# Kernel tuning notes

Hardware: AMD Instinct MI355X
Metric: run time of the kernel (lower is better)

## Reference

```python
import jax, jax.numpy as jnp
import numpy as np

N = 100000   # nodes
E = 3200000  # edges
C = 256      # in_channels
H = 64       # hidden_channels
G = 512      # graphs in batch
FC = [128, 64, 32, 16]
OUT = 2
EPS = 1e-5


def _linear(key, fan_in, fan_out):
    k1, k2 = jax.random.split(key)
    s = 1.0 / np.sqrt(fan_in)
    W = jax.random.uniform(k1, (fan_in, fan_out), jnp.float32, -s, s)
    b = jax.random.uniform(k2, (fan_out,), jnp.float32, -s, s)
    return W, b


def setup_inputs() -> dict:
    key = jax.random.key(0)
    ks = jax.random.split(key, 12)
    x = jax.random.normal(ks[0], (N, C), jnp.float32)
    edge_index = jax.random.randint(ks[1], (2, E), 0, N, dtype=jnp.int64)
    batch = jnp.sort(jax.random.randint(ks[2], (N,), 0, G, dtype=jnp.int64))
    w1, b1 = _linear(ks[3], C, H)
    w2, b2 = _linear(ks[4], H, H)
    g1 = jnp.ones((H,), jnp.float32); be1 = jnp.zeros((H,), jnp.float32)
    g2 = jnp.ones((H,), jnp.float32); be2 = jnp.zeros((H,), jnp.float32)
    fw1, fb1 = _linear(ks[5], H, FC[0])
    fw2, fb2 = _linear(ks[6], FC[0], FC[1])
    fw3, fb3 = _linear(ks[7], FC[1], FC[2])
    fw4, fb4 = _linear(ks[8], FC[2], FC[3])
    ow, ob = _linear(ks[9], FC[3], OUT)
    return dict(x=x, edge_index=edge_index, batch=batch,
                w1=w1, b1=b1, w2=w2, b2=b2,
                g1=g1, be1=be1, g2=g2, be2=be2,
                fw1=fw1, fb1=fb1, fw2=fw2, fb2=fb2,
                fw3=fw3, fb3=fb3, fw4=fw4, fb4=fb4,
                ow=ow, ob=ob)


def _gcn_layers(x, edge_index, w1, b1, w2, b2, g1, be1, g2, be2):
    # PyG GCNConv: add self loops, symmetric deg^-1/2 normalization, scatter-add at dst
    loops = jnp.arange(N, dtype=edge_index.dtype)
    src = jnp.concatenate([edge_index[0], loops])
    dst = jnp.concatenate([edge_index[1], loops])
    deg = jax.ops.segment_sum(jnp.ones((E + N,), jnp.float32), dst, num_segments=N)
    dis = jnp.where(deg > 0, jax.lax.rsqrt(jnp.maximum(deg, 1.0)), 0.0)
    norm = (dis[src] * dis[dst])[:, None]  # [E+N, 1]

    def conv(h, W, b):
        h = h @ W
        return jax.ops.segment_sum(h[src] * norm, dst, num_segments=N) + b

    def bn(h, g, be):  # BatchNorm1d over node dim (training-mode batch stats)
        m = jnp.mean(h, axis=0)
        v = jnp.var(h, axis=0)
        return (h - m) * jax.lax.rsqrt(v + EPS) * g + be

    h = bn(jax.nn.relu(conv(x, w1, b1)), g1, be1)   # dropout = identity (eval)
    h = bn(jax.nn.relu(conv(h, w2, b2)), g2, be2)
    return h


def reference(x, edge_index, batch, w1, b1, w2, b2, g1, be1, g2, be2,
              fw1, fb1, fw2, fb2, fw3, fb3, fw4, fb4, ow, ob):
    h = _gcn_layers(x, edge_index, w1, b1, w2, b2, g1, be1, g2, be2)
    # global_mean_pool over batch vector
    s = jax.ops.segment_sum(h, batch, num_segments=G)
    cnt = jax.ops.segment_sum(jnp.ones((N,), jnp.float32), batch, num_segments=G)
    p = s / jnp.maximum(cnt, 1.0)[:, None]  # [G, H]
    h = jax.nn.relu(p @ fw1 + fb1)
    h = jax.nn.relu(h @ fw2 + fb2)
    h = jax.nn.relu(h @ fw3 + fb3)
    h = jax.nn.relu(h @ fw4 + fb4)
    return h @ ow + ob  # [G, OUT]
```

## Files before the change

kernel.cpp:

```cpp
#include <hip/hip_runtime.h>
#include <hip/hip_fp16.h>

#define N_NODES 100000
#define E_EDGES 3200000
#define NG      512
#define BN_EPS  1e-5f

#define BSH     7
#define BNODES  128
#define NBUCK   782
#define NCHUNK  1024
#define CHUNK   3125

__global__ __launch_bounds__(256) void k_zero(float* __restrict__ stats1,
                                              float* __restrict__ stats2,
                                              float* __restrict__ sums,
                                              float* __restrict__ cnt) {
  int i = blockIdx.x * 256 + threadIdx.x;
  if (i < 128) { stats1[i] = 0.f; stats2[i] = 0.f; }
  if (i < NG * 64) sums[i] = 0.f;
  if (i < NG) cnt[i] = 0.f;
}

__global__ __launch_bounds__(256) void kb_hist(const int* __restrict__ ei,
                                               int* __restrict__ counts) {
  __shared__ int h[NBUCK];
  const int c = blockIdx.x, tid = threadIdx.x;
  for (int b = tid; b < NBUCK; b += 256) h[b] = 0;
  __syncthreads();
  const int* dst = ei + E_EDGES + c * CHUNK;
  for (int i = tid; i < CHUNK; i += 256) atomicAdd(&h[dst[i] >> BSH], 1);
  __syncthreads();
  for (int b = tid; b < NBUCK; b += 256) counts[b * NCHUNK + c] = h[b];
}

__global__ __launch_bounds__(1024) void kb_scan1(int* __restrict__ counts,
                                                 int* __restrict__ btot) {
  __shared__ int sm[NCHUNK];
  const int b = blockIdx.x, tid = threadIdx.x;
  const int cval = counts[b * NCHUNK + tid];
  int val = cval;
  sm[tid] = val;
  __syncthreads();
  for (int off = 1; off < NCHUNK; off <<= 1) {
    int t = (tid >= off) ? sm[tid - off] : 0;
    __syncthreads();
    val += t;
    sm[tid] = val;
    __syncthreads();
  }
  counts[b * NCHUNK + tid] = val - cval;
  if (tid == NCHUNK - 1) btot[b] = val;
}

__global__ __launch_bounds__(1024) void kb_scan2(const int* __restrict__ btot,
                                                 int* __restrict__ bbase) {
  __shared__ int sm[1024];
  const int tid = threadIdx.x;
  const int cval = (tid < NBUCK) ? btot[tid] : 0;
  int val = cval;
  sm[tid] = val;
  __syncthreads();
  for (int off = 1; off < 1024; off <<= 1) {
    int t = (tid >= off) ? sm[tid - off] : 0;
    __syncthreads();
    val += t;
    sm[tid] = val;
    __syncthreads();
  }
  if (tid < NBUCK) bbase[tid] = val - cval;
  if (tid == NBUCK - 1) bbase[NBUCK] = val;
}

__global__ __launch_bounds__(256) void kb_scatter(const int* __restrict__ ei,
                                                  const int* __restrict__ counts,
                                                  const int* __restrict__ bbase,
                                                  int* __restrict__ binned) {
  __shared__ int cur[NBUCK];
  const int c = blockIdx.x, tid = threadIdx.x;
  for (int b = tid; b < NBUCK; b += 256) cur[b] = bbase[b] + counts[b * NCHUNK + c];
  __syncthreads();
  const int* srcp = ei + c * CHUNK;
  const int* dstp = ei + E_EDGES + c * CHUNK;
  for (int i = tid; i < CHUNK; i += 256) {
    const int s = srcp[i], d = dstp[i];
    const int pos = atomicAdd(&cur[d >> BSH], 1);
    binned[pos] = ((d & (BNODES - 1)) << 17) | s;
  }
}

__global__ __launch_bounds__(256) void kb_degsort(const int* __restrict__ binned,
                                                  const int* __restrict__ bbase,
                                                  int* __restrict__ csr,
                                                  int* __restrict__ row_start,
                                                  float* __restrict__ dis) {
  __shared__ int h[BNODES];
  __shared__ int pre[BNODES];
  const int b = blockIdx.x, tid = threadIdx.x;
  if (tid < BNODES) h[tid] = 0;
  __syncthreads();
  const int e0 = bbase[b], e1 = bbase[b + 1];
  for (int i = e0 + tid; i < e1; i += 256) atomicAdd(&h[binned[i] >> 17], 1);
  __syncthreads();
  if (tid < BNODES) pre[tid] = h[tid];
  __syncthreads();
  for (int off = 1; off < BNODES; off <<= 1) {
    int t = (tid >= off && tid < BNODES) ? pre[tid - off] : 0;
    __syncthreads();
    if (tid < BNODES) pre[tid] += t;
    __syncthreads();
  }
  if (tid < BNODES) {
    const int n = b * BNODES + tid;
    const int ex = e0 + pre[tid] - h[tid];
    if (n < N_NODES) {
      row_start[n] = ex;
      dis[n] = rsqrtf((float)(h[tid] + 1));
    }
    h[tid] = ex;
  }
  if (b == NBUCK - 1 && tid == 0) row_start[N_NODES] = E_EDGES;
  __syncthreads();
  for (int i = e0 + tid; i < e1; i += 256) {
    const int v = binned[i];
    const int pos = atomicAdd(&h[v >> 17], 1);
    csr[pos] = v & 0x1FFFF;
  }
}

template <int K, bool BN>
__global__ __launch_bounds__(256) void k_gemm(const float* __restrict__ in,
                                              const float* __restrict__ W,
                                              const float* __restrict__ dis,
                                              const float* __restrict__ stats,
                                              const float* __restrict__ gam,
                                              const float* __restrict__ bet,
                                              __half* __restrict__ y) {
  __shared__ float xs[64 * 68];
  __shared__ float wsm[64 * 64];
  __shared__ float scv[64], shv[64];
  const int tid = threadIdx.x;
  const int n0 = blockIdx.x * 64;
  const int lane = tid & 63, wv = tid >> 6;
  const int nq = lane & 15;
  const int chb = wv * 16 + (lane >> 4) * 4;
  if (BN) {
    if (tid < 64) {
      const float m = stats[tid] * (1.0f / N_NODES);
      const float v = stats[64 + tid] * (1.0f / N_NODES) - m * m;
      const float sc = rsqrtf(v + BN_EPS) * gam[tid];
      scv[tid] = sc;
      shv[tid] = bet[tid] - m * sc;
    }
  }
  float a[4][4] = {{0,0,0,0},{0,0,0,0},{0,0,0,0},{0,0,0,0}};
  for (int c0 = 0; c0 < K; c0 += 64) {
    __syncthreads();
#pragma unroll
    for (int i = 0; i < 4; ++i) {
      const int idx = tid + i * 256;
      const int n = idx >> 4, c4 = (idx & 15) * 4;
      const int nn = min(n0 + n, N_NODES - 1);
      float4 v = *(const float4*)&in[(size_t)nn * K + c0 + c4];
      if (BN) {
        v.x = v.x * scv[c4] + shv[c4];
        v.y = v.y * scv[c4 + 1] + shv[c4 + 1];
        v.z = v.z * scv[c4 + 2] + shv[c4 + 2];
        v.w = v.w * scv[c4 + 3] + shv[c4 + 3];
      }
      *(float4*)&xs[n * 68 + c4] = v;
    }
#pragma unroll
    for (int i = 0; i < 4; ++i) {
      const int idx = tid + i * 256;
      const int c = idx >> 4, ch4 = (idx & 15) * 4;
      *(float4*)&wsm[c * 64 + ch4] = *(const float4*)&W[(size_t)(c0 + c) * 64 + ch4];
    }
    __syncthreads();
    for (int c = 0; c < 64; c += 4) {
      float wq[4][4];
#pragma unroll
      for (int cc = 0; cc < 4; ++cc) {
        const float4 w4 = *(const float4*)&wsm[(c + cc) * 64 + chb];
        wq[cc][0] = w4.x; wq[cc][1] = w4.y; wq[cc][2] = w4.z; wq[cc][3] = w4.w;
      }
#pragma unroll
      for (int i = 0; i < 4; ++i) {
        const float4 xv = *(const float4*)&xs[(nq + 16 * i) * 68 + c];
#pragma unroll
        for (int j = 0; j < 4; ++j) {
          a[i][j] = fmaf(xv.x, wq[0][j],
                    fmaf(xv.y, wq[1][j],
                    fmaf(xv.z, wq[2][j],
                    fmaf(xv.w, wq[3][j], a[i][j]))));
        }
      }
    }
  }
#pragma unroll
  for (int i = 0; i < 4; ++i) {
    const int n = n0 + nq + 16 * i;
    if (n < N_NODES) {
      const float d = dis[n];
      union { __half h[4]; float2 f; } u;
      u.h[0] = __float2half_rn(d * a[i][0]);
      u.h[1] = __float2half_rn(d * a[i][1]);
      u.h[2] = __float2half_rn(d * a[i][2]);
      u.h[3] = __float2half_rn(d * a[i][3]);
      *(float2*)&y[(size_t)n * 64 + chb] = u.f;
    }
  }
}

template <bool POOL>
__global__ __launch_bounds__(256) void k_gather(const int* __restrict__ csr,
                                                const int* __restrict__ rs,
                                                const __half* __restrict__ y,
                                                const float* __restrict__ dis,
                                                const float* __restrict__ bias,
                                                float* __restrict__ hout,
                                                float* __restrict__ stats,
                                                const int* __restrict__ batch,
                                                float* __restrict__ sums,
                                                float* __restrict__ cnt) {
  const int tid = threadIdx.x;
  const int lane = tid & 63;
  const int p = lane >> 5;
  const int c = lane & 31;
  const int wid = (blockIdx.x * 256 + tid) >> 6;
  const int nw = (gridDim.x * 256) >> 6;
  const int per = (N_NODES + nw - 1) / nw;
  const int n0 = wid * per;
  const int n1 = min(N_NODES, n0 + per);
  const float bx = bias[2 * c], by = bias[2 * c + 1];
  float s1x = 0.f, s1y = 0.f, s2x = 0.f, s2y = 0.f;
  int curg = -1, run = 0;
  float px = 0.f, py = 0.f;
  for (int n = n0; n < n1; ++n) {
    int e = rs[n];
    const int end = rs[n + 1];
    float ax = 0.f, ay = 0.f;
    if (p == 0) {
      const float2 f = __half22float2(*(const __half2*)&y[(size_t)n * 64 + 2 * c]);
      ax = f.x; ay = f.y;
    }
    for (; e + 8 <= end; e += 8) {
      const int i0 = csr[e + p];
      const int i1 = csr[e + 2 + p];
      const int i2 = csr[e + 4 + p];
      const int i3 = csr[e + 6 + p];
      const float2 f0 = __half22float2(*(const __half2*)&y[(size_t)i0 * 64 + 2 * c]);
      const float2 f1 = __half22float2(*(const __half2*)&y[(size_t)i1 * 64 + 2 * c]);
      const float2 f2 = __half22float2(*(const __half2*)&y[(size_t)i2 * 64 + 2 * c]);
      const float2 f3 = __half22float2(*(const __half2*)&y[(size_t)i3 * 64 + 2 * c]);
      ax += (f0.x + f1.x) + (f2.x + f3.x);
      ay += (f0.y + f1.y) + (f2.y + f3.y);
    }
    for (; e + 2 <= end; e += 2) {
      const int i0 = csr[e + p];
      const float2 f = __half22float2(*(const __half2*)&y[(size_t)i0 * 64 + 2 * c]);
      ax += f.x; ay += f.y;
    }
    if (e < end && p == 0) {
      const int i0 = csr[e];
      const float2 f = __half22float2(*(const __half2*)&y[(size_t)i0 * 64 + 2 * c]);
      ax += f.x; ay += f.y;
    }
    ax += __shfl_xor(ax, 32);
    ay += __shfl_xor(ay, 32);
    const float d = dis[n];
    const float vx = fmaxf(d * ax + bx, 0.f);
    const float vy = fmaxf(d * ay + by, 0.f);
    if (lane < 32) {
      if (!POOL) *(float2*)&hout[(size_t)n * 64 + 2 * c] = make_float2(vx, vy);
      s1x += vx; s1y += vy;
      s2x += vx * vx; s2y += vy * vy;
    }
    if (POOL) {
      const int g = batch[n];
      if (g != curg) {
        if (run) {
          if (lane < 32) {
            atomicAdd(&sums[curg * 64 + 2 * c], px);
            atomicAdd(&sums[curg * 64 + 2 * c + 1], py);
          }
          if (lane == 0) atomicAdd(&cnt[curg], (float)run);
        }
        curg = g; run = 0; px = 0.f; py = 0.f;
      }
      if (lane < 32) { px += vx; py += vy; }
      ++run;
    }
  }
  if (POOL && run) {
    if (lane < 32) {
      atomicAdd(&sums[curg * 64 + 2 * c], px);
      atomicAdd(&sums[curg * 64 + 2 * c + 1], py);
    }
    if (lane == 0) atomicAdd(&cnt[curg], (float)run);
  }
  __shared__ float r1[256], r2[256];
  const int wv = tid >> 6;
  if (lane < 32) {
    r1[wv * 64 + 2 * c] = s1x; r1[wv * 64 + 2 * c + 1] = s1y;
    r2[wv * 64 + 2 * c] = s2x; r2[wv * 64 + 2 * c + 1] = s2y;
  }
  __syncthreads();
  if (tid < 64) {
    atomicAdd(&stats[tid], r1[tid] + r1[tid + 64] + r1[tid + 128] + r1[tid + 192]);
  } else if (tid < 128) {
    const int h = tid - 64;
    atomicAdd(&stats[64 + h], r2[h] + r2[h + 64] + r2[h + 128] + r2[h + 192]);
  }
}

__global__ __launch_bounds__(128) void k_mlp(const float* __restrict__ sums,
                                             const float* __restrict__ cnt,
                                             const float* __restrict__ stats,
                                             const float* __restrict__ gam,
                                             const float* __restrict__ bet,
                                             const float* __restrict__ fw1, const float* __restrict__ fb1,
                                             const float* __restrict__ fw2, const float* __restrict__ fb2,
                                             const float* __restrict__ fw3, const float* __restrict__ fb3,
                                             const float* __restrict__ fw4, const float* __restrict__ fb4,
                                             const float* __restrict__ ow, const float* __restrict__ ob,
                                             float* __restrict__ out) {
  __shared__ float u0[128], u1[128];
  const int g = blockIdx.x, t = threadIdx.x;
  if (t < 64) {
    const float m = stats[t] * (1.0f / N_NODES);
    const float v = stats[64 + t] * (1.0f / N_NODES) - m * m;
    const float sc = rsqrtf(v + BN_EPS) * gam[t];
    const float sh = bet[t] - m * sc;
    u0[t] = (sums[g * 64 + t] / fmaxf(cnt[g], 1.0f)) * sc + sh;
  }
  __syncthreads();
  if (t < 128) {
    float a = fb1[t];
    for (int k = 0; k < 64; ++k) a = fmaf(u0[k], fw1[k * 128 + t], a);
    u1[t] = fmaxf(a, 0.f);
  }
  __syncthreads();
  if (t < 64) {
    float a = fb2[t];
    for (int k = 0; k < 128; ++k) a = fmaf(u1[k], fw2[k * 64 + t], a);
    u0[t] = fmaxf(a, 0.f);
  }
  __syncthreads();
  if (t < 32) {
    float a = fb3[t];
    for (int k = 0; k < 64; ++k) a = fmaf(u0[k], fw3[k * 32 + t], a);
    u1[t] = fmaxf(a, 0.f);
  }
  __syncthreads();
  if (t < 16) {
    float a = fb4[t];
    for (int k = 0; k < 32; ++k) a = fmaf(u1[k], fw4[k * 16 + t], a);
    u0[t] = fmaxf(a, 0.f);
  }
  __syncthreads();
  if (t < 2) {
    float a = ob[t];
    for (int k = 0; k < 16; ++k) a = fmaf(u0[k], ow[k * 2 + t], a);
    out[g * 2 + t] = a;
  }
}

extern "C" void kernel_launch(void* const* d_in, const int* in_sizes, int n_in,
                              void* d_out, int out_size, void* d_ws, size_t ws_size,
                              hipStream_t stream) {
  const float* x    = (const float*)d_in[0];
  const int*   ei   = (const int*)d_in[1];
  const int*   batch= (const int*)d_in[2];
  const float* w1   = (const float*)d_in[3];
  const float* b1   = (const float*)d_in[4];
  const float* w2   = (const float*)d_in[5];
  const float* b2   = (const float*)d_in[6];
  const float* g1   = (const float*)d_in[7];
  const float* be1  = (const float*)d_in[8];
  const float* g2   = (const float*)d_in[9];
  const float* be2  = (const float*)d_in[10];
  const float* fw1  = (const float*)d_in[11]; const float* fb1 = (const float*)d_in[12];
  const float* fw2  = (const float*)d_in[13]; const float* fb2 = (const float*)d_in[14];
  const float* fw3  = (const float*)d_in[15]; const float* fb3 = (const float*)d_in[16];
  const float* fw4  = (const float*)d_in[17]; const float* fb4 = (const float*)d_in[18];
  const float* ow   = (const float*)d_in[19]; const float* ob  = (const float*)d_in[20];
  float* out = (float*)d_out;

  char* ws = (char*)d_ws;
  auto alloc = [&](size_t bytes) {
    void* p = ws;
    ws += (bytes + 255) & ~(size_t)255;
    return p;
  };
  float*  dis      = (float*)alloc((size_t)N_NODES * 4);
  int*    counts   = (int*)  alloc((size_t)NBUCK * NCHUNK * 4);
  int*    btot     = (int*)  alloc((size_t)NBUCK * 4);
  int*    bbase    = (int*)  alloc((size_t)(NBUCK + 1) * 4);
  int*    binned   = (int*)  alloc((size_t)E_EDGES * 4);
  int*    csr      = (int*)  alloc((size_t)E_EDGES * 4);
  int*    row_start= (int*)  alloc((size_t)(N_NODES + 1) * 4);
  __half* yH       = (__half*)alloc((size_t)N_NODES * 64 * 2);
  float*  hB       = (float*)alloc((size_t)N_NODES * 64 * 4);
  float*  stats1   = (float*)alloc(512);
  float*  stats2   = (float*)alloc(512);
  float*  sums     = (float*)alloc((size_t)NG * 64 * 4);
  float*  cnt      = (float*)alloc((size_t)NG * 4);

  const int nblkG = (N_NODES + 63) / 64;

  k_zero    <<<128, 256, 0, stream>>>(stats1, stats2, sums, cnt);
  kb_hist   <<<NCHUNK, 256, 0, stream>>>(ei, counts);
  kb_scan1  <<<NBUCK, NCHUNK, 0, stream>>>(counts, btot);
  kb_scan2  <<<1, 1024, 0, stream>>>(btot, bbase);
  kb_scatter<<<NCHUNK, 256, 0, stream>>>(ei, counts, bbase, binned);
  kb_degsort<<<NBUCK, 256, 0, stream>>>(binned, bbase, csr, row_start, dis);

  k_gemm<256, false><<<nblkG, 256, 0, stream>>>(x, w1, dis, nullptr, nullptr, nullptr, yH);
  k_gather<false><<<2048, 256, 0, stream>>>(csr, row_start, yH, dis, b1, hB, stats1,
                                            nullptr, nullptr, nullptr);

  k_gemm<64, true><<<nblkG, 256, 0, stream>>>(hB, w2, dis, stats1, g1, be1, yH);
  k_gather<true><<<2048, 256, 0, stream>>>(csr, row_start, yH, dis, b2, nullptr, stats2,
                                           batch, sums, cnt);

  k_mlp<<<NG, 128, 0, stream>>>(sums, cnt, stats2, g2, be2,
                                fw1, fb1, fw2, fb2, fw3, fb3, fw4, fb4, ow, ob, out);
}
```

Measured before the change: 601.9 us.

## Replace per-chunk count scan with global atomic bucket cursors and LDS-staged degree sort

The edge bucketing pipeline drops the per-chunk counts matrix and its 782-block scan kernel. Per-bucket totals are now accumulated with global atomics, and each scatter block reserves its ranges through an atomic cursor after recounting its own chunk. Chunks are larger (256 instead of 1024). The per-bucket sort stages edges in LDS when a bucket fits, so CSR writes become coalesced. The cost is a second histogram pass in the scatter kernel and nondeterministic edge order within a bucket, which can change float summation order.

```diff
diff --git a/kernel.cpp b/kernel.cpp
--- a/kernel.cpp
+++ b/kernel.cpp
@@ -9,21 +9,24 @@
 #define BSH     7
 #define BNODES  128
 #define NBUCK   782
-#define NCHUNK  1024
-#define CHUNK   3125
-
-__global__ __launch_bounds__(256) void k_zero(float* __restrict__ stats1,
+#define NCHUNK  256
+#define CHUNK   12500
+#define DCAP    5120
+
+__global__ __launch_bounds__(256) void k_zero(int* __restrict__ btot,
+                                              float* __restrict__ stats1,
                                               float* __restrict__ stats2,
                                               float* __restrict__ sums,
                                               float* __restrict__ cnt) {
   int i = blockIdx.x * 256 + threadIdx.x;
+  if (i < NBUCK) btot[i] = 0;
   if (i < 128) { stats1[i] = 0.f; stats2[i] = 0.f; }
   if (i < NG * 64) sums[i] = 0.f;
   if (i < NG) cnt[i] = 0.f;
 }
 
 __global__ __launch_bounds__(256) void kb_hist(const int* __restrict__ ei,
-                                               int* __restrict__ counts) {
+                                               int* __restrict__ btot) {
   __shared__ int h[NBUCK];
   const int c = blockIdx.x, tid = threadIdx.x;
   for (int b = tid; b < NBUCK; b += 256) h[b] = 0;
@@ -31,30 +34,13 @@
   const int* dst = ei + E_EDGES + c * CHUNK;
   for (int i = tid; i < CHUNK; i += 256) atomicAdd(&h[dst[i] >> BSH], 1);
   __syncthreads();
-  for (int b = tid; b < NBUCK; b += 256) counts[b * NCHUNK + c] = h[b];
-}
-
-__global__ __launch_bounds__(1024) void kb_scan1(int* __restrict__ counts,
-                                                 int* __restrict__ btot) {
-  __shared__ int sm[NCHUNK];
-  const int b = blockIdx.x, tid = threadIdx.x;
-  const int cval = counts[b * NCHUNK + tid];
-  int val = cval;
-  sm[tid] = val;
-  __syncthreads();
-  for (int off = 1; off < NCHUNK; off <<= 1) {
-    int t = (tid >= off) ? sm[tid - off] : 0;
-    __syncthreads();
-    val += t;
-    sm[tid] = val;
-    __syncthreads();
-  }
-  counts[b * NCHUNK + tid] = val - cval;
-  if (tid == NCHUNK - 1) btot[b] = val;
+  for (int b = tid; b < NBUCK; b += 256)
+    if (h[b]) atomicAdd(&btot[b], h[b]);
 }
 
 __global__ __launch_bounds__(1024) void kb_scan2(const int* __restrict__ btot,
-                                                 int* __restrict__ bbase) {
+                                                 int* __restrict__ bbase,
+                                                 int* __restrict__ cursor) {
   __shared__ int sm[1024];
   const int tid = threadIdx.x;
   const int cval = (tid < NBUCK) ? btot[tid] : 0;
@@ -68,24 +54,31 @@
     sm[tid] = val;
     __syncthreads();
   }
-  if (tid < NBUCK) bbase[tid] = val - cval;
+  if (tid < NBUCK) { bbase[tid] = val - cval; cursor[tid] = val - cval; }
   if (tid == NBUCK - 1) bbase[NBUCK] = val;
 }
 
 __global__ __launch_bounds__(256) void kb_scatter(const int* __restrict__ ei,
-                                                  const int* __restrict__ counts,
-                                                  const int* __restrict__ bbase,
+                                                  int* __restrict__ cursor,
                                                   int* __restrict__ binned) {
-  __shared__ int cur[NBUCK];
+  __shared__ int cnt[NBUCK], lcur[NBUCK], res[NBUCK];
   const int c = blockIdx.x, tid = threadIdx.x;
-  for (int b = tid; b < NBUCK; b += 256) cur[b] = bbase[b] + counts[b * NCHUNK + c];
+  for (int b = tid; b < NBUCK; b += 256) cnt[b] = 0;
   __syncthreads();
   const int* srcp = ei + c * CHUNK;
   const int* dstp = ei + E_EDGES + c * CHUNK;
+  for (int i = tid; i < CHUNK; i += 256) atomicAdd(&cnt[dstp[i] >> BSH], 1);
+  __syncthreads();
+  for (int b = tid; b < NBUCK; b += 256) {
+    res[b] = cnt[b] ? atomicAdd(&cursor[b], cnt[b]) : 0;
+    lcur[b] = 0;
+  }
+  __syncthreads();
   for (int i = tid; i < CHUNK; i += 256) {
     const int s = srcp[i], d = dstp[i];
-    const int pos = atomicAdd(&cur[d >> BSH], 1);
-    binned[pos] = ((d & (BNODES - 1)) << 17) | s;
+    const int b = d >> BSH;
+    const int slot = atomicAdd(&lcur[b], 1);
+    binned[res[b] + slot] = ((d & (BNODES - 1)) << 17) | s;
   }
 }
 
@@ -94,13 +87,25 @@
                                                   int* __restrict__ csr,
                                                   int* __restrict__ row_start,
                                                   float* __restrict__ dis) {
+  __shared__ int sA[DCAP];
+  __shared__ int sB[DCAP];
   __shared__ int h[BNODES];
   __shared__ int pre[BNODES];
+  __shared__ int cur[BNODES];
   const int b = blockIdx.x, tid = threadIdx.x;
+  const int e0 = bbase[b], e1 = bbase[b + 1];
+  const int sz = e1 - e0;
   if (tid < BNODES) h[tid] = 0;
   __syncthreads();
-  const int e0 = bbase[b], e1 = bbase[b + 1];
-  for (int i = e0 + tid; i < e1; i += 256) atomicAdd(&h[binned[i] >> 17], 1);
+  if (sz <= DCAP) {
+    for (int i = tid; i < sz; i += 256) {
+      const int v = binned[e0 + i];
+      sA[i] = v;
+      atomicAdd(&h[v >> 17], 1);
+    }
+  } else {
+    for (int i = e0 + tid; i < e1; i += 256) atomicAdd(&h[binned[i] >> 17], 1);
+  }
   __syncthreads();
   if (tid < BNODES) pre[tid] = h[tid];
   __syncthreads();
@@ -111,20 +116,30 @@
     __syncthreads();
   }
   if (tid < BNODES) {
+    const int ex = pre[tid] - h[tid];
     const int n = b * BNODES + tid;
-    const int ex = e0 + pre[tid] - h[tid];
     if (n < N_NODES) {
-      row_start[n] = ex;
+      row_start[n] = e0 + ex;
       dis[n] = rsqrtf((float)(h[tid] + 1));
     }
-    h[tid] = ex;
+    cur[tid] = ex;
   }
   if (b == NBUCK - 1 && tid == 0) row_start[N_NODES] = E_EDGES;
   __syncthreads();
-  for (int i = e0 + tid; i < e1; i += 256) {
-    const int v = binned[i];
-    const int pos = atomicAdd(&h[v >> 17], 1);
-    csr[pos] = v & 0x1FFFF;
+  if (sz <= DCAP) {
+    for (int i = tid; i < sz; i += 256) {
+      const int v = sA[i];
+      const int pos = atomicAdd(&cur[v >> 17], 1);
+      sB[pos] = v & 0x1FFFF;
+    }
+    __syncthreads();
+    for (int i = tid; i < sz; i += 256) csr[e0 + i] = sB[i];
+  } else {
+    for (int i = e0 + tid; i < e1; i += 256) {
+      const int v = binned[i];
+      const int pos = atomicAdd(&cur[v >> 17], 1);
+      csr[e0 + pos] = v & 0x1FFFF;
+    }
   }
 }
 
@@ -394,9 +409,9 @@
     return p;
   };
   float*  dis      = (float*)alloc((size_t)N_NODES * 4);
-  int*    counts   = (int*)  alloc((size_t)NBUCK * NCHUNK * 4);
   int*    btot     = (int*)  alloc((size_t)NBUCK * 4);
   int*    bbase    = (int*)  alloc((size_t)(NBUCK + 1) * 4);
+  int*    cursor   = (int*)  alloc((size_t)NBUCK * 4);
   int*    binned   = (int*)  alloc((size_t)E_EDGES * 4);
   int*    csr      = (int*)  alloc((size_t)E_EDGES * 4);
   int*    row_start= (int*)  alloc((size_t)(N_NODES + 1) * 4);
@@ -409,11 +424,10 @@
 
   const int nblkG = (N_NODES + 63) / 64;
 
-  k_zero    <<<128, 256, 0, stream>>>(stats1, stats2, sums, cnt);
-  kb_hist   <<<NCHUNK, 256, 0, stream>>>(ei, counts);
-  kb_scan1  <<<NBUCK, NCHUNK, 0, stream>>>(counts, btot);
-  kb_scan2  <<<1, 1024, 0, stream>>>(btot, bbase);
-  kb_scatter<<<NCHUNK, 256, 0, stream>>>(ei, counts, bbase, binned);
+  k_zero    <<<128, 256, 0, stream>>>(btot, stats1, stats2, sums, cnt);
+  kb_hist   <<<NCHUNK, 256, 0, stream>>>(ei, btot);
+  kb_scan2  <<<1, 1024, 0, stream>>>(btot, bbase, cursor);
+  kb_scatter<<<NCHUNK, 256, 0, stream>>>(ei, cursor, binned);
   kb_degsort<<<NBUCK, 256, 0, stream>>>(binned, bbase, csr, row_start, dis);
 
   k_gemm<256, false><<<nblkG, 256, 0, stream>>>(x, w1, dis, nullptr, nullptr, nullptr, yH);
```

After: 610.3 us. No clear change (+1.4%).
